# Kernel optimization log

Hardware: AMD Instinct MI355X
Metric: run time of the kernel (lower is better)

The kernel has to match this reference:

```python
import jax, jax.numpy as jnp
import numpy as np

SIGMA = 2.5
NEIGH_THRESH = 8.0
COORD_SCALE = 40.0  # Angstrom-scale box so the 8A cutoff gives realistic sparsity


def _rbf_weights(vs, vg):
    # vs: [B, Ns, 3], vg: [B, Ng, 3] -> [B, Ns, Ng] row-normalized gaussian RBF
    d2 = (jnp.sum(vs * vs, -1)[:, :, None]
          + jnp.sum(vg * vg, -1)[:, None, :]
          - 2.0 * jnp.einsum('bnd,bmd->bnm', vs, vg))
    d2 = jnp.maximum(d2, 0.0)
    w = jnp.exp(-d2 / (SIGMA ** 2)) * (d2 < NEIGH_THRESH ** 2)
    return w / (jnp.sum(w, -1, keepdims=True) + 1e-8)


def setup_inputs() -> dict:
    key = jax.random.key(0)
    ks = jax.random.split(key, 12)
    B, Ns, Ng, D = 4, 16384, 2048, 128
    s = 1.0 / np.sqrt(D)
    sp = 1.0 / np.sqrt(2 * D)
    return {
        'xs': jax.random.normal(ks[0], (B, Ns, D), jnp.float32),
        'xg': jax.random.normal(ks[1], (B, Ng, D), jnp.float32),
        'vs': jax.random.uniform(ks[2], (B, Ns, 3), jnp.float32) * COORD_SCALE,
        'vg': jax.random.uniform(ks[3], (B, Ng, 3), jnp.float32) * COORD_SCALE,
        'Ws_pre': jax.random.normal(ks[4], (D, D), jnp.float32) * s,
        'bs_pre': jnp.zeros((D,), jnp.float32),
        'Wg_pre': jax.random.normal(ks[5], (D, D), jnp.float32) * s,
        'bg_pre': jnp.zeros((D,), jnp.float32),
        'Ws_post': jax.random.normal(ks[6], (2 * D, D), jnp.float32) * sp,
        'bs_post': jnp.zeros((D,), jnp.float32),
        'Wg_post': jax.random.normal(ks[7], (2 * D, D), jnp.float32) * sp,
        'bg_post': jnp.zeros((D,), jnp.float32),
    }


def reference(xs, xg, vs, vg, Ws_pre, bs_pre, Wg_pre, bg_pre,
              Ws_post, bs_post, Wg_post, bg_post):
    # pre-encoders (surface.x = s_pre_block(surface.x); graph.x = g_pre_block(graph.x))
    xs_h = jax.nn.relu(jnp.einsum('bnd,de->bne', xs, Ws_pre) + bs_pre)
    xg_h = jax.nn.relu(jnp.einsum('bmd,de->bme', xg, Wg_pre) + bg_pre)
    # RBF bipartite message passing (non-BP path): xs_out = rbf_w @ graph.x; xg_out = rbf_w.T @ surface.x
    w = _rbf_weights(vs, vg)                                  # [B, Ns, Ng]
    xs_out = jnp.einsum('bnm,bmd->bnd', w, xg_h)              # graph -> surface
    xg_out = jnp.einsum('bnm,bnd->bmd', w, xs_h)              # surface -> graph
    # post blocks fuse old features with messages
    xs_new = jax.nn.relu(jnp.einsum('bnd,de->bne',
                                    jnp.concatenate([xs_h, xs_out], -1), Ws_post) + bs_post)
    xg_new = jax.nn.relu(jnp.einsum('bmd,de->bme',
                                    jnp.concatenate([xg_h, xg_out], -1), Wg_post) + bg_post)
    # concat along node dim so output is a single array: [B, Ns+Ng, D]
    return jnp.concatenate([xs_new, xg_new], axis=1)
```

## Files before the change

kernel.cpp:

```cpp
#include <hip/hip_runtime.h>
#include <hip/hip_bf16.h>

#define BB 4
#define NS 16384
#define NG 2048
#define DD 128
#define SPLITG 16
#define C2 (-0.23083120f)

typedef short bf16x8 __attribute__((ext_vector_type(8)));
typedef unsigned short u16x8 __attribute__((ext_vector_type(8)));
typedef float f32x4 __attribute__((ext_vector_type(4)));
typedef float f32x16 __attribute__((ext_vector_type(16)));
typedef int i32x4 __attribute__((ext_vector_type(4)));

#if __has_builtin(__builtin_amdgcn_exp2f)
#define EXP2(x) __builtin_amdgcn_exp2f(x)
#else
#define EXP2(x) exp2f(x)
#endif

__device__ __forceinline__ unsigned short f2bf(float x) {
  unsigned int u = __builtin_bit_cast(unsigned int, x);
  u += 0x7FFFu + ((u >> 16) & 1u);
  return (unsigned short)(u >> 16);
}
__device__ __forceinline__ float bf2f(unsigned short h) {
  unsigned int u = ((unsigned int)h) << 16;
  return __builtin_bit_cast(float, u);
}

#define PACK_SWAP(e0, e1, e2, e3, e4, e5, e6, e7, OUT)                       \
  {                                                                          \
    unsigned pq0, pq1, pq2, pq3;                                             \
    asm("v_cvt_pk_bf16_f32 %0, %1, %2" : "=v"(pq0) : "v"(e0), "v"(e1));      \
    asm("v_cvt_pk_bf16_f32 %0, %1, %2" : "=v"(pq1) : "v"(e2), "v"(e3));      \
    asm("v_cvt_pk_bf16_f32 %0, %1, %2" : "=v"(pq2) : "v"(e4), "v"(e5));      \
    asm("v_cvt_pk_bf16_f32 %0, %1, %2" : "=v"(pq3) : "v"(e6), "v"(e7));      \
    asm("v_permlane32_swap_b32 %0, %1" : "+v"(pq0), "+v"(pq2));              \
    asm("v_permlane32_swap_b32 %0, %1" : "+v"(pq1), "+v"(pq3));              \
    i32x4 tmp_ = {(int)pq0, (int)pq1, (int)pq2, (int)pq3};                   \
    OUT = __builtin_bit_cast(bf16x8, tmp_);                                  \
  }

__device__ __forceinline__ void posprep1(const float* __restrict__ v, int i,
                                         unsigned short* __restrict__ pos1,
                                         unsigned short* __restrict__ pos2) {
  float x = v[i * 3 + 0], y = v[i * 3 + 1], z = v[i * 3 + 2];
  unsigned short hx = f2bf(x), hy = f2bf(y), hz = f2bf(z);
  float fx = bf2f(hx), fy = bf2f(hy), fz = bf2f(hz);
  unsigned short lx = f2bf(x - fx), ly = f2bf(y - fy), lz = f2bf(z - fz);
  float n = x * x + y * y + z * z;
  unsigned short nh = f2bf(n);
  unsigned short nl = f2bf(n - bf2f(nh));
  unsigned short m2hx = f2bf(-2.f * fx), m2hy = f2bf(-2.f * fy),
                 m2hz = f2bf(-2.f * fz);
  unsigned short m2lx = f2bf(-2.f * bf2f(lx)), m2ly = f2bf(-2.f * bf2f(ly)),
                 m2lz = f2bf(-2.f * bf2f(lz));
  const unsigned short one = 0x3F80;
  u16x8 a0 = {m2hx, m2hy, m2hz, m2lx, m2ly, m2lz, m2hx, m2hy};
  u16x8 a1 = {m2hz, m2lx, m2ly, m2lz, nh, nl, one, one};
  u16x8 b0 = {hx, hy, hz, hx, hy, hz, lx, ly};
  u16x8 b1 = {lz, lx, ly, lz, one, one, nh, nl};
  *(u16x8*)(pos1 + (long)i * 16) = a0;
  *(u16x8*)(pos1 + (long)i * 16 + 8) = a1;
  *(u16x8*)(pos2 + (long)i * 16) = b0;
  *(u16x8*)(pos2 + (long)i * 16 + 8) = b1;
}

__global__ __launch_bounds__(256) void prep_k(
    const float* __restrict__ vs, const float* __restrict__ vg,
    const float* __restrict__ Ws_pre, const float* __restrict__ Wg_pre,
    const float* __restrict__ Ws_post, const float* __restrict__ Wg_post,
    unsigned short* __restrict__ pos1_s, unsigned short* __restrict__ pos2_s,
    unsigned short* __restrict__ pos1_g, unsigned short* __restrict__ pos2_g,
    unsigned short* __restrict__ WtS_pre, unsigned short* __restrict__ WtG_pre,
    unsigned short* __restrict__ WtS_post,
    unsigned short* __restrict__ WtG_post) {
  const int NODEBLK = (BB * (NS + NG)) / 256;
  int bid = blockIdx.x, tid = threadIdx.x;
  if (bid < NODEBLK) {
    int i = bid * 256 + tid;
    if (i < BB * NS)
      posprep1(vs, i, pos1_s, pos2_s);
    else
      posprep1(vg, i - BB * NS, pos1_g, pos2_g);
  } else {
    int k2 = (bid - NODEBLK) * 256 + tid;
    const float* W;
    unsigned short* Wt;
    int kshift, loc;
    if (k2 < 16384) { W = Ws_pre; Wt = WtS_pre; kshift = 7; loc = k2; }
    else if (k2 < 32768) { W = Wg_pre; Wt = WtG_pre; kshift = 7; loc = k2 - 16384; }
    else if (k2 < 65536) { W = Ws_post; Wt = WtS_post; kshift = 8; loc = k2 - 32768; }
    else { W = Wg_post; Wt = WtG_post; kshift = 8; loc = k2 - 65536; }
    int K = 1 << kshift;
    int e = loc >> kshift, k = loc & (K - 1);
    Wt[(long)e * K + k] = f2bf(W[(long)k * 128 + e]);
  }
}

__global__ __launch_bounds__(256) void pre_mfma_k(
    const float* __restrict__ xs, const float* __restrict__ xg,
    const unsigned short* __restrict__ WtS,
    const unsigned short* __restrict__ WtG, const float* __restrict__ bs,
    const float* __restrict__ bg, unsigned short* __restrict__ xs_h,
    unsigned short* __restrict__ xg_h) {
  long r0 = (long)blockIdx.x * 64;
  const float* X;
  const unsigned short* Wt;
  const float* bias;
  unsigned short* H;
  long row0;
  if (r0 < (long)BB * NS) {
    X = xs; Wt = WtS; bias = bs; H = xs_h; row0 = r0;
  } else {
    X = xg; Wt = WtG; bias = bg; H = xg_h; row0 = r0 - (long)BB * NS;
  }
  int tid = threadIdx.x, l = tid & 63, w = tid >> 6;
  int g = l >> 4, r = l & 15;
  row0 += w * 16;
  const float* xrow = X + (row0 + r) * DD;
  f32x4 z4 = {0.f, 0.f, 0.f, 0.f};
  f32x4 acc[8];
#pragma unroll
  for (int i = 0; i < 8; ++i) acc[i] = z4;
#pragma unroll
  for (int ks = 0; ks < 4; ++ks) {
    float4 v0 = *(const float4*)(xrow + ks * 32 + 8 * g);
    float4 v1 = *(const float4*)(xrow + ks * 32 + 8 * g + 4);
    bf16x8 a;
    a[0] = (short)f2bf(v0.x); a[1] = (short)f2bf(v0.y);
    a[2] = (short)f2bf(v0.z); a[3] = (short)f2bf(v0.w);
    a[4] = (short)f2bf(v1.x); a[5] = (short)f2bf(v1.y);
    a[6] = (short)f2bf(v1.z); a[7] = (short)f2bf(v1.w);
#pragma unroll
    for (int ct = 0; ct < 8; ++ct) {
      bf16x8 b = *reinterpret_cast<const bf16x8*>(Wt + (ct * 16 + r) * DD +
                                                  ks * 32 + 8 * g);
      acc[ct] = __builtin_amdgcn_mfma_f32_16x16x32_bf16(a, b, acc[ct], 0, 0, 0);
    }
  }
#pragma unroll
  for (int ct = 0; ct < 8; ++ct) {
    float bv = bias[ct * 16 + r];
#pragma unroll
    for (int r4 = 0; r4 < 4; ++r4) {
      long row = row0 + 4 * g + r4;
      H[row * DD + ct * 16 + r] = f2bf(fmaxf(acc[ct][r4] + bv, 0.f));
    }
  }
}

__global__ __launch_bounds__(256) void transpose_k(
    const unsigned short* __restrict__ H, unsigned short* __restrict__ HT,
    int R, const float* __restrict__ scale) {
  __shared__ unsigned short lds[64 * 136];
  int tid = threadIdx.x;
  long r0 = (long)blockIdx.x * 64;
#pragma unroll
  for (int q = 0; q < 4; ++q) {
    int idx = q * 2048 + tid * 8;
    int rr = idx >> 7, cc = idx & 127;
    u16x8 v = *reinterpret_cast<const u16x8*>(H + (r0 + rr) * 128 + cc);
    if (scale) {
      float s = scale[r0 + rr];
#pragma unroll
      for (int i = 0; i < 8; ++i) v[i] = f2bf(bf2f(v[i]) * s);
    }
    *(u16x8*)&lds[rr * 136 + cc] = v;
  }
  __syncthreads();
  int e = tid >> 1, half = tid & 1;
#pragma unroll
  for (int q = 0; q < 4; ++q) {
    u16x8 v;
#pragma unroll
    for (int i = 0; i < 8; ++i)
      v[i] = lds[(half * 32 + q * 8 + i) * 136 + e];
    *reinterpret_cast<u16x8*>(HT + (long)e * R + r0 + half * 32 + q * 8) = v;
  }
}

__global__ __launch_bounds__(256) void msg_s_k(
    const unsigned short* __restrict__ pos1_g,
    const unsigned short* __restrict__ pos2_s,
    const unsigned short* __restrict__ xg_hT, unsigned short* __restrict__ xs_o,
    float* __restrict__ rsinv) {
  __shared__ __align__(16) unsigned short ldsB[2][128 * 64];
  const int tid = threadIdx.x;
  const int w = tid >> 6, l = tid & 63;
  const int ln = l & 31, hi = l >> 5;
  const int b = blockIdx.y;
  const long bNS = (long)b * NS, bNG = (long)b * NG;
  const long row0 = (long)blockIdx.x * 128 + w * 32;
  const long BNG = (long)BB * NG;
  const int NCH = NG / 64;

  const bf16x8 bP = *reinterpret_cast<const bf16x8*>(
      pos2_s + (bNS + row0 + ln) * 16 + 8 * hi);

  const f32x16 zz = {0.f, 0.f, 0.f, 0.f, 0.f, 0.f, 0.f, 0.f,
                     0.f, 0.f, 0.f, 0.f, 0.f, 0.f, 0.f, 0.f};
  f32x16 acc[4] = {zz, zz, zz, zz};
  float rs0 = 0.f, rs1 = 0.f, rs2 = 0.f, rs3 = 0.f;

  const int tf = tid >> 3;
  const int tsp = tid & 7;
  const unsigned short* p0 = xg_hT + (long)(0 * 32 + tf) * BNG + bNG +
                             (tsp ^ (tf & 7)) * 8;
  const unsigned short* p1 = p0 + (long)32 * BNG;
  const unsigned short* p2 = p0 + (long)64 * BNG;
  const unsigned short* p3 = p0 + (long)96 * BNG;
  const unsigned short* pp = pos1_g + (bNG + ln) * 16 + 8 * hi;

  u16x8 stA[4];
  bf16x8 pA0, pA1, pA0n, pA1n;
  stA[0] = *reinterpret_cast<const u16x8*>(p0);
  stA[1] = *reinterpret_cast<const u16x8*>(p1);
  stA[2] = *reinterpret_cast<const u16x8*>(p2);
  stA[3] = *reinterpret_cast<const u16x8*>(p3);
#pragma unroll
  for (int q = 0; q < 4; ++q)
    *(u16x8*)&ldsB[0][(q * 32 + tf) * 64 + tsp * 8] = stA[q];
  stA[0] = *reinterpret_cast<const u16x8*>(p0 + 64);
  stA[1] = *reinterpret_cast<const u16x8*>(p1 + 64);
  stA[2] = *reinterpret_cast<const u16x8*>(p2 + 64);
  stA[3] = *reinterpret_cast<const u16x8*>(p3 + 64);
  p0 += 128; p1 += 128; p2 += 128; p3 += 128;
  pA0 = *reinterpret_cast<const bf16x8*>(pp);
  pA1 = *reinterpret_cast<const bf16x8*>(pp + 32 * 16);
  pA0n = *reinterpret_cast<const bf16x8*>(pp + 64 * 16);
  pA1n = *reinterpret_cast<const bf16x8*>(pp + 96 * 16);
  pp += 128 * 16;
  __syncthreads();

#pragma unroll 1
  for (int c = 0; c < NCH; ++c) {
    const int buf = c & 1;
    float ex[2][16];
    bf16x8 fr[2][2];
#pragma unroll
    for (int t2 = 0; t2 < 2; ++t2) {
      f32x16 S = __builtin_amdgcn_mfma_f32_32x32x16_bf16(t2 ? pA1 : pA0, bP,
                                                         zz, 0, 0, 0);
#pragma unroll
      for (int r = 0; r < 16; ++r) ex[t2][r] = EXP2(S[r] * C2);
      PACK_SWAP(ex[t2][0], ex[t2][1], ex[t2][2], ex[t2][3], ex[t2][4],
                ex[t2][5], ex[t2][6], ex[t2][7], fr[t2][0]);
      PACK_SWAP(ex[t2][8], ex[t2][9], ex[t2][10], ex[t2][11], ex[t2][12],
                ex[t2][13], ex[t2][14], ex[t2][15], fr[t2][1]);
    }
#pragma unroll
    for (int r = 0; r < 4; ++r) {
      rs0 += ex[0][r] + ex[1][r];
      rs1 += ex[0][r + 4] + ex[1][r + 4];
      rs2 += ex[0][r + 8] + ex[1][r + 8];
      rs3 += ex[0][r + 12] + ex[1][r + 12];
    }
#pragma unroll
    for (int t2 = 0; t2 < 2; ++t2) {
#pragma unroll
      for (int kh = 0; kh < 2; ++kh) {
        const int kt = t2 * 2 + kh;
        const int spr = ((kt * 2 + hi) ^ (ln & 7)) * 8;
#pragma unroll
        for (int nt = 0; nt < 4; ++nt) {
          const bf16x8 bm = *reinterpret_cast<const bf16x8*>(
              &ldsB[buf][(nt * 32 + ln) * 64 + spr]);
          acc[nt] = __builtin_amdgcn_mfma_f32_32x32x16_bf16(fr[t2][kh], bm,
                                                            acc[nt], 0, 0, 0);
        }
      }
    }
    if (c + 1 < NCH) {
#pragma unroll
      for (int q = 0; q < 4; ++q)
        *(u16x8*)&ldsB[buf ^ 1][(q * 32 + tf) * 64 + tsp * 8] = stA[q];
    }
    if (c + 2 < NCH) {
      stA[0] = *reinterpret_cast<const u16x8*>(p0);
      stA[1] = *reinterpret_cast<const u16x8*>(p1);
      stA[2] = *reinterpret_cast<const u16x8*>(p2);
      stA[3] = *reinterpret_cast<const u16x8*>(p3);
      p0 += 64; p1 += 64; p2 += 64; p3 += 64;
    }
    pA0 = pA0n;
    pA1 = pA1n;
    if (c + 2 < NCH) {
      pA0n = *reinterpret_cast<const bf16x8*>(pp);
      pA1n = *reinterpret_cast<const bf16x8*>(pp + 32 * 16);
      pp += 64 * 16;
    }
    __syncthreads();
  }

  float rtot = (rs0 + rs1) + (rs2 + rs3);
  rtot += __shfl_xor(rtot, 32, 64);
  float denom = rtot + 1e-8f;
  float rsi = 1.f / denom;
  if (hi == 0) rsinv[bNS + row0 + ln] = rsi;
#pragma unroll
  for (int r = 0; r < 16; ++r) {
    const int crow = (r & 3) + 8 * (r >> 2) + 4 * hi;
    float rsib = __shfl(rsi, crow, 64);
    long rowg = bNS + row0 + crow;
#pragma unroll
    for (int nt = 0; nt < 4; ++nt)
      xs_o[rowg * DD + nt * 32 + ln] = f2bf(acc[nt][r] * rsib);
  }
}

__global__ __launch_bounds__(256) void msg_g_k(
    const unsigned short* __restrict__ pos1_s,
    const unsigned short* __restrict__ pos2_g,
    const unsigned short* __restrict__ xs_hT, unsigned short* __restrict__ part) {
  __shared__ __align__(16) unsigned short ldsB[2][128 * 64];
  const int tid = threadIdx.x;
  const int w = tid >> 6, l = tid & 63;
  const int ln = l & 31, hi = l >> 5;
  const int b = blockIdx.y, spz = blockIdx.z;
  const long bNS = (long)b * NS, bNG = (long)b * NG;
  const long nbeg = (long)spz * (NS / SPLITG);
  const long row0 = (long)blockIdx.x * 128 + w * 32;
  const long BNS = (long)BB * NS;
  const int NCH = (NS / SPLITG) / 64;

  const bf16x8 bP = *reinterpret_cast<const bf16x8*>(
      pos2_g + (bNG + row0 + ln) * 16 + 8 * hi);

  const f32x16 zz = {0.f, 0.f, 0.f, 0.f, 0.f, 0.f, 0.f, 0.f,
                     0.f, 0.f, 0.f, 0.f, 0.f, 0.f, 0.f, 0.f};
  f32x16 acc[4] = {zz, zz, zz, zz};

  const int tf = tid >> 3;
  const int tsp = tid & 7;
  const unsigned short* p0 = xs_hT + (long)(0 * 32 + tf) * BNS + bNS + nbeg +
                             (tsp ^ (tf & 7)) * 8;
  const unsigned short* p1 = p0 + (long)32 * BNS;
  const unsigned short* p2 = p0 + (long)64 * BNS;
  const unsigned short* p3 = p0 + (long)96 * BNS;
  const unsigned short* pp = pos1_s + (bNS + nbeg + ln) * 16 + 8 * hi;

  u16x8 stA[4];
  bf16x8 pA0, pA1, pA0n, pA1n;
  stA[0] = *reinterpret_cast<const u16x8*>(p0);
  stA[1] = *reinterpret_cast<const u16x8*>(p1);
  stA[2] = *reinterpret_cast<const u16x8*>(p2);
  stA[3] = *reinterpret_cast<const u16x8*>(p3);
#pragma unroll
  for (int q = 0; q < 4; ++q)
    *(u16x8*)&ldsB[0][(q * 32 + tf) * 64 + tsp * 8] = stA[q];
  stA[0] = *reinterpret_cast<const u16x8*>(p0 + 64);
  stA[1] = *reinterpret_cast<const u16x8*>(p1 + 64);
  stA[2] = *reinterpret_cast<const u16x8*>(p2 + 64);
  stA[3] = *reinterpret_cast<const u16x8*>(p3 + 64);
  p0 += 128; p1 += 128; p2 += 128; p3 += 128;
  pA0 = *reinterpret_cast<const bf16x8*>(pp);
  pA1 = *reinterpret_cast<const bf16x8*>(pp + 32 * 16);
  pA0n = *reinterpret_cast<const bf16x8*>(pp + 64 * 16);
  pA1n = *reinterpret_cast<const bf16x8*>(pp + 96 * 16);
  pp += 128 * 16;
  __syncthreads();

#pragma unroll 1
  for (int c = 0; c < NCH; ++c) {
    const int buf = c & 1;
    float ex[2][16];
    bf16x8 fr[2][2];
#pragma unroll
    for (int t2 = 0; t2 < 2; ++t2) {
      f32x16 S = __builtin_amdgcn_mfma_f32_32x32x16_bf16(t2 ? pA1 : pA0, bP,
                                                         zz, 0, 0, 0);
#pragma unroll
      for (int r = 0; r < 16; ++r) ex[t2][r] = EXP2(S[r] * C2);
      PACK_SWAP(ex[t2][0], ex[t2][1], ex[t2][2], ex[t2][3], ex[t2][4],
                ex[t2][5], ex[t2][6], ex[t2][7], fr[t2][0]);
      PACK_SWAP(ex[t2][8], ex[t2][9], ex[t2][10], ex[t2][11], ex[t2][12],
                ex[t2][13], ex[t2][14], ex[t2][15], fr[t2][1]);
    }
#pragma unroll
    for (int t2 = 0; t2 < 2; ++t2) {
#pragma unroll
      for (int kh = 0; kh < 2; ++kh) {
        const int kt = t2 * 2 + kh;
        const int spr = ((kt * 2 + hi) ^ (ln & 7)) * 8;
#pragma unroll
        for (int nt = 0; nt < 4; ++nt) {
          const bf16x8 bm = *reinterpret_cast<const bf16x8*>(
              &ldsB[buf][(nt * 32 + ln) * 64 + spr]);
          acc[nt] = __builtin_amdgcn_mfma_f32_32x32x16_bf16(fr[t2][kh], bm,
                                                            acc[nt], 0, 0, 0);
        }
      }
    }
    if (c + 1 < NCH) {
#pragma unroll
      for (int q = 0; q < 4; ++q)
        *(u16x8*)&ldsB[buf ^ 1][(q * 32 + tf) * 64 + tsp * 8] = stA[q];
    }
    if (c + 2 < NCH) {
      stA[0] = *reinterpret_cast<const u16x8*>(p0);
      stA[1] = *reinterpret_cast<const u16x8*>(p1);
      stA[2] = *reinterpret_cast<const u16x8*>(p2);
      stA[3] = *reinterpret_cast<const u16x8*>(p3);
      p0 += 64; p1 += 64; p2 += 64; p3 += 64;
    }
    pA0 = pA0n;
    pA1 = pA1n;
    if (c + 2 < NCH) {
      pA0n = *reinterpret_cast<const bf16x8*>(pp);
      pA1n = *reinterpret_cast<const bf16x8*>(pp + 32 * 16);
      pp += 64 * 16;
    }
    __syncthreads();
  }

  const long pbase = (long)spz * BB * NG;
#pragma unroll
  for (int r = 0; r < 16; ++r) {
    const int crow = (r & 3) + 8 * (r >> 2) + 4 * hi;
    long rowg = pbase + bNG + row0 + crow;
#pragma unroll
    for (int nt = 0; nt < 4; ++nt)
      part[rowg * DD + nt * 32 + ln] = f2bf(acc[nt][r]);
  }
}

__global__ __launch_bounds__(256) void reduce_k(
    const unsigned short* __restrict__ part, unsigned short* __restrict__ xg_o) {
  long i = ((long)blockIdx.x * 256 + threadIdx.x) * 8;
  const long S = (long)BB * NG * DD;
  float a[8];
#pragma unroll
  for (int k = 0; k < 8; ++k) a[k] = 0.f;
#pragma unroll
  for (int s = 0; s < SPLITG; ++s) {
    u16x8 v = *reinterpret_cast<const u16x8*>(part + s * S + i);
#pragma unroll
    for (int k = 0; k < 8; ++k) a[k] += bf2f(v[k]);
  }
  u16x8 o;
#pragma unroll
  for (int k = 0; k < 8; ++k) o[k] = f2bf(a[k]);
  *reinterpret_cast<u16x8*>(xg_o + i) = o;
}

__global__ __launch_bounds__(256) void post_mfma_k(
    const unsigned short* __restrict__ Ha, const unsigned short* __restrict__ Hb,
    const unsigned short* __restrict__ Wt, const float* __restrict__ bias,
    float* __restrict__ out, int shift, int mask, int off) {
  int tid = threadIdx.x, l = tid & 63, w = tid >> 6;
  int g = l >> 4, r = l & 15;
  long row0 = (long)blockIdx.x * 64 + w * 16;
  const unsigned short* ha = Ha + (row0 + r) * DD;
  const unsigned short* hb = Hb + (row0 + r) * DD;
  f32x4 z4 = {0.f, 0.f, 0.f, 0.f};
  f32x4 acc[8];
#pragma unroll
  for (int i = 0; i < 8; ++i) acc[i] = z4;
#pragma unroll
  for (int ks = 0; ks < 8; ++ks) {
    const unsigned short* src = (ks < 4) ? (ha + ks * 32) : (hb + (ks - 4) * 32);
    bf16x8 a = *reinterpret_cast<const bf16x8*>(src + 8 * g);
#pragma unroll
    for (int ct = 0; ct < 8; ++ct) {
      bf16x8 b = *reinterpret_cast<const bf16x8*>(Wt + (ct * 16 + r) * 256 +
                                                  ks * 32 + 8 * g);
      acc[ct] = __builtin_amdgcn_mfma_f32_16x16x32_bf16(a, b, acc[ct], 0, 0, 0);
    }
  }
#pragma unroll
  for (int ct = 0; ct < 8; ++ct) {
    float bv = bias[ct * 16 + r];
#pragma unroll
    for (int r4 = 0; r4 < 4; ++r4) {
      long rowg = row0 + 4 * g + r4;
      long bb = rowg >> shift;
      long n = rowg & mask;
      out[(bb * (NS + NG) + off + n) * DD + ct * 16 + r] =
          fmaxf(acc[ct][r4] + bv, 0.f);
    }
  }
}

extern "C" void kernel_launch(void* const* d_in, const int* in_sizes, int n_in,
                              void* d_out, int out_size, void* d_ws,
                              size_t ws_size, hipStream_t stream) {
  const float* xs = (const float*)d_in[0];
  const float* xg = (const float*)d_in[1];
  const float* vs = (const float*)d_in[2];
  const float* vg = (const float*)d_in[3];
  const float* Ws_pre = (const float*)d_in[4];
  const float* bs_pre = (const float*)d_in[5];
  const float* Wg_pre = (const float*)d_in[6];
  const float* bg_pre = (const float*)d_in[7];
  const float* Ws_post = (const float*)d_in[8];
  const float* bs_post = (const float*)d_in[9];
  const float* Wg_post = (const float*)d_in[10];
  const float* bg_post = (const float*)d_in[11];
  float* out = (float*)d_out;

  char* p = (char*)d_ws;
  unsigned short* pos1_s = (unsigned short*)p; p += (size_t)BB * NS * 16 * 2;
  unsigned short* pos2_s = (unsigned short*)p; p += (size_t)BB * NS * 16 * 2;
  unsigned short* pos1_g = (unsigned short*)p; p += (size_t)BB * NG * 16 * 2;
  unsigned short* pos2_g = (unsigned short*)p; p += (size_t)BB * NG * 16 * 2;
  unsigned short* WtS_pre = (unsigned short*)p; p += (size_t)128 * 128 * 2;
  unsigned short* WtG_pre = (unsigned short*)p; p += (size_t)128 * 128 * 2;
  unsigned short* WtS_post = (unsigned short*)p; p += (size_t)128 * 256 * 2;
  unsigned short* WtG_post = (unsigned short*)p; p += (size_t)128 * 256 * 2;
  unsigned short* xg_h = (unsigned short*)p; p += (size_t)BB * NG * DD * 2;
  unsigned short* xg_hT = (unsigned short*)p; p += (size_t)BB * NG * DD * 2;
  unsigned short* xs_hT = (unsigned short*)p; p += (size_t)BB * NS * DD * 2;
  unsigned short* xg_o = (unsigned short*)p; p += (size_t)BB * NG * DD * 2;
  float* rsinv = (float*)p; p += (size_t)BB * NS * 4;
  unsigned short* xs_h = (unsigned short*)p;
  unsigned short* xs_o = xs_h + (size_t)BB * NS * DD;
  unsigned short* part = xs_h;
  p += (size_t)2 * BB * NS * DD * 2;

  prep_k<<<(BB * (NS + NG)) / 256 + 98304 / 256, 256, 0, stream>>>(
      vs, vg, Ws_pre, Wg_pre, Ws_post, Wg_post, pos1_s, pos2_s, pos1_g,
      pos2_g, WtS_pre, WtG_pre, WtS_post, WtG_post);
  pre_mfma_k<<<(BB * NS + BB * NG) / 64, 256, 0, stream>>>(
      xs, xg, WtS_pre, WtG_pre, bs_pre, bg_pre, xs_h, xg_h);
  transpose_k<<<BB * NG / 64, 256, 0, stream>>>(xg_h, xg_hT, BB * NG, nullptr);
  msg_s_k<<<dim3(NS / 128, BB), 256, 0, stream>>>(pos1_g, pos2_s, xg_hT, xs_o,
                                                  rsinv);
  transpose_k<<<BB * NS / 64, 256, 0, stream>>>(xs_h, xs_hT, BB * NS, rsinv);
  post_mfma_k<<<BB * NS / 64, 256, 0, stream>>>(xs_h, xs_o, WtS_post, bs_post,
                                                out, 14, NS - 1, 0);
  msg_g_k<<<dim3(NG / 128, BB, SPLITG), 256, 0, stream>>>(pos1_s, pos2_g,
                                                          xs_hT, part);
  reduce_k<<<(BB * NG * DD) / 8 / 256, 256, 0, stream>>>(part, xg_o);
  post_mfma_k<<<BB * NG / 64, 256, 0, stream>>>(xg_h, xg_o, WtG_post, bg_post,
                                                out, 11, NG - 1, NS);
}
```

Before: 198.4 us.

## Split surface message kernel over graph dimension with combine pass

Splits msg_s_k's loop over the graph nodes into two z-slices. Each slice writes unnormalized bf16 partial messages and partial row sums, and a new combine kernel adds the two halves and applies the normalization. The goal is more blocks in flight and shorter per-block serial loops, which should improve GPU occupancy and latency hiding. The cost is an extra kernel launch plus an extra global read/write pass over the surface message buffer, and the partials are rounded to bf16 before being summed.

```diff
diff --git a/kernel.cpp b/kernel.cpp
--- a/kernel.cpp
+++ b/kernel.cpp
@@ -6,7 +6,8 @@
 #define NG 2048
 #define DD 128
 #define SPLITG 16
-#define C2 (-0.23083120f)
+#define SPLITS 2
+#define C2F (-0.23083120f)
 
 typedef short bf16x8 __attribute__((ext_vector_type(8)));
 typedef unsigned short u16x8 __attribute__((ext_vector_type(8)));
@@ -185,17 +186,19 @@
 __global__ __launch_bounds__(256) void msg_s_k(
     const unsigned short* __restrict__ pos1_g,
     const unsigned short* __restrict__ pos2_s,
-    const unsigned short* __restrict__ xg_hT, unsigned short* __restrict__ xs_o,
-    float* __restrict__ rsinv) {
+    const unsigned short* __restrict__ xg_hT,
+    unsigned short* __restrict__ part0, unsigned short* __restrict__ part1,
+    float* __restrict__ rs_part) {
   __shared__ __align__(16) unsigned short ldsB[2][128 * 64];
   const int tid = threadIdx.x;
   const int w = tid >> 6, l = tid & 63;
   const int ln = l & 31, hi = l >> 5;
-  const int b = blockIdx.y;
+  const int b = blockIdx.y, spz = blockIdx.z;
   const long bNS = (long)b * NS, bNG = (long)b * NG;
+  const long nbeg = (long)spz * (NG / SPLITS);
   const long row0 = (long)blockIdx.x * 128 + w * 32;
   const long BNG = (long)BB * NG;
-  const int NCH = NG / 64;
+  const int NCH = (NG / SPLITS) / 64;
 
   const bf16x8 bP = *reinterpret_cast<const bf16x8*>(
       pos2_s + (bNS + row0 + ln) * 16 + 8 * hi);
@@ -207,12 +210,12 @@
 
   const int tf = tid >> 3;
   const int tsp = tid & 7;
-  const unsigned short* p0 = xg_hT + (long)(0 * 32 + tf) * BNG + bNG +
+  const unsigned short* p0 = xg_hT + (long)tf * BNG + bNG + nbeg +
                              (tsp ^ (tf & 7)) * 8;
   const unsigned short* p1 = p0 + (long)32 * BNG;
   const unsigned short* p2 = p0 + (long)64 * BNG;
   const unsigned short* p3 = p0 + (long)96 * BNG;
-  const unsigned short* pp = pos1_g + (bNG + ln) * 16 + 8 * hi;
+  const unsigned short* pp = pos1_g + (bNG + nbeg + ln) * 16 + 8 * hi;
 
   u16x8 stA[4];
   bf16x8 pA0, pA1, pA0n, pA1n;
@@ -245,7 +248,7 @@
       f32x16 S = __builtin_amdgcn_mfma_f32_32x32x16_bf16(t2 ? pA1 : pA0, bP,
                                                          zz, 0, 0, 0);
 #pragma unroll
-      for (int r = 0; r < 16; ++r) ex[t2][r] = EXP2(S[r] * C2);
+      for (int r = 0; r < 16; ++r) ex[t2][r] = EXP2(S[r] * C2F);
       PACK_SWAP(ex[t2][0], ex[t2][1], ex[t2][2], ex[t2][3], ex[t2][4],
                 ex[t2][5], ex[t2][6], ex[t2][7], fr[t2][0]);
       PACK_SWAP(ex[t2][8], ex[t2][9], ex[t2][10], ex[t2][11], ex[t2][12],
@@ -295,20 +298,34 @@
     __syncthreads();
   }
 
-  float rtot = (rs0 + rs1) + (rs2 + rs3);
-  rtot += __shfl_xor(rtot, 32, 64);
-  float denom = rtot + 1e-8f;
-  float rsi = 1.f / denom;
-  if (hi == 0) rsinv[bNS + row0 + ln] = rsi;
+  float rsp = (rs0 + rs1) + (rs2 + rs3);
+  rsp += __shfl_xor(rsp, 32, 64);
+  if (hi == 0) rs_part[(long)spz * (BB * NS) + bNS + row0 + ln] = rsp;
+  unsigned short* dst = spz ? part1 : part0;
 #pragma unroll
   for (int r = 0; r < 16; ++r) {
     const int crow = (r & 3) + 8 * (r >> 2) + 4 * hi;
-    float rsib = __shfl(rsi, crow, 64);
     long rowg = bNS + row0 + crow;
 #pragma unroll
     for (int nt = 0; nt < 4; ++nt)
-      xs_o[rowg * DD + nt * 32 + ln] = f2bf(acc[nt][r] * rsib);
-  }
+      dst[rowg * DD + nt * 32 + ln] = f2bf(acc[nt][r]);
+  }
+}
+
+__global__ __launch_bounds__(256) void combine_s_k(
+    const unsigned short* __restrict__ part1, const float* __restrict__ rs_part,
+    unsigned short* __restrict__ xs_o, float* __restrict__ rsinv) {
+  long i = ((long)blockIdx.x * 256 + threadIdx.x) * 8;
+  long row = i >> 7;
+  float s = rs_part[row] + rs_part[(long)BB * NS + row] + 1e-8f;
+  float ri = 1.f / s;
+  u16x8 a = *reinterpret_cast<const u16x8*>(xs_o + i);
+  u16x8 bq = *reinterpret_cast<const u16x8*>(part1 + i);
+  u16x8 o;
+#pragma unroll
+  for (int k = 0; k < 8; ++k) o[k] = f2bf((bf2f(a[k]) + bf2f(bq[k])) * ri);
+  *reinterpret_cast<u16x8*>(xs_o + i) = o;
+  if ((i & 127) == 0) rsinv[row] = ri;
 }
 
 __global__ __launch_bounds__(256) void msg_g_k(
@@ -335,7 +352,7 @@
 
   const int tf = tid >> 3;
   const int tsp = tid & 7;
-  const unsigned short* p0 = xs_hT + (long)(0 * 32 + tf) * BNS + bNS + nbeg +
+  const unsigned short* p0 = xs_hT + (long)tf * BNS + bNS + nbeg +
                              (tsp ^ (tf & 7)) * 8;
   const unsigned short* p1 = p0 + (long)32 * BNS;
   const unsigned short* p2 = p0 + (long)64 * BNS;
@@ -373,7 +390,7 @@
       f32x16 S = __builtin_amdgcn_mfma_f32_32x32x16_bf16(t2 ? pA1 : pA0, bP,
                                                          zz, 0, 0, 0);
 #pragma unroll
-      for (int r = 0; r < 16; ++r) ex[t2][r] = EXP2(S[r] * C2);
+      for (int r = 0; r < 16; ++r) ex[t2][r] = EXP2(S[r] * C2F);
       PACK_SWAP(ex[t2][0], ex[t2][1], ex[t2][2], ex[t2][3], ex[t2][4],
                 ex[t2][5], ex[t2][6], ex[t2][7], fr[t2][0]);
       PACK_SWAP(ex[t2][8], ex[t2][9], ex[t2][10], ex[t2][11], ex[t2][12],
@@ -513,11 +530,13 @@
   unsigned short* xg_h = (unsigned short*)p; p += (size_t)BB * NG * DD * 2;
   unsigned short* xg_hT = (unsigned short*)p; p += (size_t)BB * NG * DD * 2;
   unsigned short* xs_hT = (unsigned short*)p; p += (size_t)BB * NS * DD * 2;
+  unsigned short* part1 = xs_hT;
   unsigned short* xg_o = (unsigned short*)p; p += (size_t)BB * NG * DD * 2;
   float* rsinv = (float*)p; p += (size_t)BB * NS * 4;
+  float* rs_part = (float*)p; p += (size_t)SPLITS * BB * NS * 4;
   unsigned short* xs_h = (unsigned short*)p;
   unsigned short* xs_o = xs_h + (size_t)BB * NS * DD;
-  unsigned short* part = xs_h;
+  unsigned short* part_g = xs_h;
   p += (size_t)2 * BB * NS * DD * 2;
 
   prep_k<<<(BB * (NS + NG)) / 256 + 98304 / 256, 256, 0, stream>>>(
@@ -526,14 +545,16 @@
   pre_mfma_k<<<(BB * NS + BB * NG) / 64, 256, 0, stream>>>(
       xs, xg, WtS_pre, WtG_pre, bs_pre, bg_pre, xs_h, xg_h);
   transpose_k<<<BB * NG / 64, 256, 0, stream>>>(xg_h, xg_hT, BB * NG, nullptr);
-  msg_s_k<<<dim3(NS / 128, BB), 256, 0, stream>>>(pos1_g, pos2_s, xg_hT, xs_o,
-                                                  rsinv);
+  msg_s_k<<<dim3(NS / 128, BB, SPLITS), 256, 0, stream>>>(
+      pos1_g, pos2_s, xg_hT, xs_o, part1, rs_part);
+  combine_s_k<<<(BB * NS * DD) / 8 / 256, 256, 0, stream>>>(part1, rs_part,
+                                                            xs_o, rsinv);
   transpose_k<<<BB * NS / 64, 256, 0, stream>>>(xs_h, xs_hT, BB * NS, rsinv);
   post_mfma_k<<<BB * NS / 64, 256, 0, stream>>>(xs_h, xs_o, WtS_post, bs_post,
                                                 out, 14, NS - 1, 0);
   msg_g_k<<<dim3(NG / 128, BB, SPLITG), 256, 0, stream>>>(pos1_s, pos2_g,
-                                                          xs_hT, part);
-  reduce_k<<<(BB * NG * DD) / 8 / 256, 256, 0, stream>>>(part, xg_o);
+                                                          xs_hT, part_g);
+  reduce_k<<<(BB * NG * DD) / 8 / 256, 256, 0, stream>>>(part_g, xg_o);
   post_mfma_k<<<BB * NG / 64, 256, 0, stream>>>(xg_h, xg_o, WtG_post, bg_post,
                                                 out, 11, NG - 1, NS);
 }
```

Measured after the change: 205.9 us. +3.8%, slower.

## Software-pipeline RBF weight computation one chunk ahead of aggregation MFMAs

Applied to the files above, without the earlier changes.

In both message-passing kernels, the distance MFMA, exp2 and bf16 packing for the next chunk now run interleaved with the aggregation MFMAs of the current chunk. The current chunk's fragments come from a prologue that computes the first chunk before the loop. This lets exp/VALU work overlap the matrix-core work instead of serialising with it. The pack-and-permlane sequence is also merged into one asm block with explicit s_nop hazards, and position loads now go straight from global memory each iteration instead of being double-buffered in registers. This raises register pressure and adds load latency to the critical path.

```diff
diff --git a/kernel.cpp b/kernel.cpp
--- a/kernel.cpp
+++ b/kernel.cpp
@@ -6,7 +6,7 @@
 #define NG 2048
 #define DD 128
 #define SPLITG 16
-#define C2 (-0.23083120f)
+#define C2F (-0.23083120f)
 
 typedef short bf16x8 __attribute__((ext_vector_type(8)));
 typedef unsigned short u16x8 __attribute__((ext_vector_type(8)));
@@ -30,17 +30,22 @@
   return __builtin_bit_cast(float, u);
 }
 
-#define PACK_SWAP(e0, e1, e2, e3, e4, e5, e6, e7, OUT)                       \
-  {                                                                          \
-    unsigned pq0, pq1, pq2, pq3;                                             \
-    asm("v_cvt_pk_bf16_f32 %0, %1, %2" : "=v"(pq0) : "v"(e0), "v"(e1));      \
-    asm("v_cvt_pk_bf16_f32 %0, %1, %2" : "=v"(pq1) : "v"(e2), "v"(e3));      \
-    asm("v_cvt_pk_bf16_f32 %0, %1, %2" : "=v"(pq2) : "v"(e4), "v"(e5));      \
-    asm("v_cvt_pk_bf16_f32 %0, %1, %2" : "=v"(pq3) : "v"(e6), "v"(e7));      \
-    asm("v_permlane32_swap_b32 %0, %1" : "+v"(pq0), "+v"(pq2));              \
-    asm("v_permlane32_swap_b32 %0, %1" : "+v"(pq1), "+v"(pq3));              \
-    i32x4 tmp_ = {(int)pq0, (int)pq1, (int)pq2, (int)pq3};                   \
-    OUT = __builtin_bit_cast(bf16x8, tmp_);                                  \
+#define PACK_SWAP(e0, e1, e2, e3, e4, e5, e6, e7, OUT)                        \
+  {                                                                           \
+    unsigned pq0, pq1, pq2, pq3;                                              \
+    asm("v_cvt_pk_bf16_f32 %0, %4, %5\n\t"                                    \
+        "v_cvt_pk_bf16_f32 %1, %6, %7\n\t"                                    \
+        "v_cvt_pk_bf16_f32 %2, %8, %9\n\t"                                    \
+        "v_cvt_pk_bf16_f32 %3, %10, %11\n\t"                                  \
+        "s_nop 1\n\t"                                                         \
+        "v_permlane32_swap_b32 %0, %2\n\t"                                    \
+        "v_permlane32_swap_b32 %1, %3\n\t"                                    \
+        "s_nop 1"                                                             \
+        : "=&v"(pq0), "=&v"(pq1), "=&v"(pq2), "=&v"(pq3)                      \
+        : "v"(e0), "v"(e1), "v"(e2), "v"(e3), "v"(e4), "v"(e5), "v"(e6),      \
+          "v"(e7));                                                           \
+    i32x4 tmp_ = {(int)pq0, (int)pq1, (int)pq2, (int)pq3};                    \
+    OUT = __builtin_bit_cast(bf16x8, tmp_);                                   \
   }
 
 __device__ __forceinline__ void posprep1(const float* __restrict__ v, int i,
@@ -207,15 +212,13 @@
 
   const int tf = tid >> 3;
   const int tsp = tid & 7;
-  const unsigned short* p0 = xg_hT + (long)(0 * 32 + tf) * BNG + bNG +
-                             (tsp ^ (tf & 7)) * 8;
+  const unsigned short* p0 = xg_hT + (long)tf * BNG + bNG + (tsp ^ (tf & 7)) * 8;
   const unsigned short* p1 = p0 + (long)32 * BNG;
   const unsigned short* p2 = p0 + (long)64 * BNG;
   const unsigned short* p3 = p0 + (long)96 * BNG;
   const unsigned short* pp = pos1_g + (bNG + ln) * 16 + 8 * hi;
 
   u16x8 stA[4];
-  bf16x8 pA0, pA1, pA0n, pA1n;
   stA[0] = *reinterpret_cast<const u16x8*>(p0);
   stA[1] = *reinterpret_cast<const u16x8*>(p1);
   stA[2] = *reinterpret_cast<const u16x8*>(p2);
@@ -228,55 +231,100 @@
   stA[2] = *reinterpret_cast<const u16x8*>(p2 + 64);
   stA[3] = *reinterpret_cast<const u16x8*>(p3 + 64);
   p0 += 128; p1 += 128; p2 += 128; p3 += 128;
-  pA0 = *reinterpret_cast<const bf16x8*>(pp);
-  pA1 = *reinterpret_cast<const bf16x8*>(pp + 32 * 16);
-  pA0n = *reinterpret_cast<const bf16x8*>(pp + 64 * 16);
-  pA1n = *reinterpret_cast<const bf16x8*>(pp + 96 * 16);
-  pp += 128 * 16;
+
+  bf16x8 frC0, frC1, frC2, frC3;
+  {
+    bf16x8 a0 = *reinterpret_cast<const bf16x8*>(pp);
+    f32x16 S = __builtin_amdgcn_mfma_f32_32x32x16_bf16(a0, bP, zz, 0, 0, 0);
+    float ex[16];
+#pragma unroll
+    for (int r = 0; r < 16; ++r) ex[r] = EXP2(S[r] * C2F);
+#pragma unroll
+    for (int r = 0; r < 4; ++r) {
+      rs0 += ex[r]; rs1 += ex[r + 4]; rs2 += ex[r + 8]; rs3 += ex[r + 12];
+    }
+    PACK_SWAP(ex[0], ex[1], ex[2], ex[3], ex[4], ex[5], ex[6], ex[7], frC0);
+    PACK_SWAP(ex[8], ex[9], ex[10], ex[11], ex[12], ex[13], ex[14], ex[15],
+              frC1);
+    bf16x8 a1 = *reinterpret_cast<const bf16x8*>(pp + 32 * 16);
+    S = __builtin_amdgcn_mfma_f32_32x32x16_bf16(a1, bP, zz, 0, 0, 0);
+#pragma unroll
+    for (int r = 0; r < 16; ++r) ex[r] = EXP2(S[r] * C2F);
+#pragma unroll
+    for (int r = 0; r < 4; ++r) {
+      rs0 += ex[r]; rs1 += ex[r + 4]; rs2 += ex[r + 8]; rs3 += ex[r + 12];
+    }
+    PACK_SWAP(ex[0], ex[1], ex[2], ex[3], ex[4], ex[5], ex[6], ex[7], frC2);
+    PACK_SWAP(ex[8], ex[9], ex[10], ex[11], ex[12], ex[13], ex[14], ex[15],
+              frC3);
+  }
   __syncthreads();
 
 #pragma unroll 1
   for (int c = 0; c < NCH; ++c) {
     const int buf = c & 1;
-    float ex[2][16];
-    bf16x8 fr[2][2];
-#pragma unroll
-    for (int t2 = 0; t2 < 2; ++t2) {
-      f32x16 S = __builtin_amdgcn_mfma_f32_32x32x16_bf16(t2 ? pA1 : pA0, bP,
-                                                         zz, 0, 0, 0);
-#pragma unroll
-      for (int r = 0; r < 16; ++r) ex[t2][r] = EXP2(S[r] * C2);
-      PACK_SWAP(ex[t2][0], ex[t2][1], ex[t2][2], ex[t2][3], ex[t2][4],
-                ex[t2][5], ex[t2][6], ex[t2][7], fr[t2][0]);
-      PACK_SWAP(ex[t2][8], ex[t2][9], ex[t2][10], ex[t2][11], ex[t2][12],
-                ex[t2][13], ex[t2][14], ex[t2][15], fr[t2][1]);
-    }
-#pragma unroll
-    for (int r = 0; r < 4; ++r) {
-      rs0 += ex[0][r] + ex[1][r];
-      rs1 += ex[0][r + 4] + ex[1][r + 4];
-      rs2 += ex[0][r + 8] + ex[1][r + 8];
-      rs3 += ex[0][r + 12] + ex[1][r + 12];
-    }
-#pragma unroll
-    for (int t2 = 0; t2 < 2; ++t2) {
-#pragma unroll
-      for (int kh = 0; kh < 2; ++kh) {
-        const int kt = t2 * 2 + kh;
-        const int spr = ((kt * 2 + hi) ^ (ln & 7)) * 8;
-#pragma unroll
-        for (int nt = 0; nt < 4; ++nt) {
-          const bf16x8 bm = *reinterpret_cast<const bf16x8*>(
-              &ldsB[buf][(nt * 32 + ln) * 64 + spr]);
-          acc[nt] = __builtin_amdgcn_mfma_f32_32x32x16_bf16(fr[t2][kh], bm,
-                                                            acc[nt], 0, 0, 0);
-        }
+    const bool haveN = (c + 1 < NCH);
+    bf16x8 frN0, frN1, frN2, frN3;
+    f32x16 S;
+    if (haveN) {
+      bf16x8 a0 =
+          *reinterpret_cast<const bf16x8*>(pp + (long)(c + 1) * 1024);
+      S = __builtin_amdgcn_mfma_f32_32x32x16_bf16(a0, bP, zz, 0, 0, 0);
+    }
+#pragma unroll
+    for (int kt = 0; kt < 2; ++kt) {
+      const bf16x8 fA = kt ? frC1 : frC0;
+      const int spr = ((kt * 2 + hi) ^ (ln & 7)) * 8;
+#pragma unroll
+      for (int nt = 0; nt < 4; ++nt) {
+        const bf16x8 bm = *reinterpret_cast<const bf16x8*>(
+            &ldsB[buf][(nt * 32 + ln) * 64 + spr]);
+        acc[nt] =
+            __builtin_amdgcn_mfma_f32_32x32x16_bf16(fA, bm, acc[nt], 0, 0, 0);
       }
     }
-    if (c + 1 < NCH) {
+    if (haveN) {
+      float ex[16];
+#pragma unroll
+      for (int r = 0; r < 16; ++r) ex[r] = EXP2(S[r] * C2F);
+#pragma unroll
+      for (int r = 0; r < 4; ++r) {
+        rs0 += ex[r]; rs1 += ex[r + 4]; rs2 += ex[r + 8]; rs3 += ex[r + 12];
+      }
+      PACK_SWAP(ex[0], ex[1], ex[2], ex[3], ex[4], ex[5], ex[6], ex[7], frN0);
+      PACK_SWAP(ex[8], ex[9], ex[10], ex[11], ex[12], ex[13], ex[14], ex[15],
+                frN1);
+      bf16x8 a1 = *reinterpret_cast<const bf16x8*>(pp + (long)(c + 1) * 1024 +
+                                                   32 * 16);
+      S = __builtin_amdgcn_mfma_f32_32x32x16_bf16(a1, bP, zz, 0, 0, 0);
+    }
+#pragma unroll
+    for (int kt = 2; kt < 4; ++kt) {
+      const bf16x8 fA = (kt == 2) ? frC2 : frC3;
+      const int spr = ((kt * 2 + hi) ^ (ln & 7)) * 8;
+#pragma unroll
+      for (int nt = 0; nt < 4; ++nt) {
+        const bf16x8 bm = *reinterpret_cast<const bf16x8*>(
+            &ldsB[buf][(nt * 32 + ln) * 64 + spr]);
+        acc[nt] =
+            __builtin_amdgcn_mfma_f32_32x32x16_bf16(fA, bm, acc[nt], 0, 0, 0);
+      }
+    }
+    if (haveN) {
+      float ex[16];
+#pragma unroll
+      for (int r = 0; r < 16; ++r) ex[r] = EXP2(S[r] * C2F);
+#pragma unroll
+      for (int r = 0; r < 4; ++r) {
+        rs0 += ex[r]; rs1 += ex[r + 4]; rs2 += ex[r + 8]; rs3 += ex[r + 12];
+      }
+      PACK_SWAP(ex[0], ex[1], ex[2], ex[3], ex[4], ex[5], ex[6], ex[7], frN2);
+      PACK_SWAP(ex[8], ex[9], ex[10], ex[11], ex[12], ex[13], ex[14], ex[15],
+                frN3);
 #pragma unroll
       for (int q = 0; q < 4; ++q)
         *(u16x8*)&ldsB[buf ^ 1][(q * 32 + tf) * 64 + tsp * 8] = stA[q];
+      frC0 = frN0; frC1 = frN1; frC2 = frN2; frC3 = frN3;
     }
     if (c + 2 < NCH) {
       stA[0] = *reinterpret_cast<const u16x8*>(p0);
@@ -284,13 +332,6 @@
       stA[2] = *reinterpret_cast<const u16x8*>(p2);
       stA[3] = *reinterpret_cast<const u16x8*>(p3);
       p0 += 64; p1 += 64; p2 += 64; p3 += 64;
-    }
-    pA0 = pA0n;
-    pA1 = pA1n;
-    if (c + 2 < NCH) {
-      pA0n = *reinterpret_cast<const bf16x8*>(pp);
-      pA1n = *reinterpret_cast<const bf16x8*>(pp + 32 * 16);
-      pp += 64 * 16;
     }
     __syncthreads();
   }
@@ -335,7 +376,7 @@
 
   const int tf = tid >> 3;
   const int tsp = tid & 7;
-  const unsigned short* p0 = xs_hT + (long)(0 * 32 + tf) * BNS + bNS + nbeg +
+  const unsigned short* p0 = xs_hT + (long)tf * BNS + bNS + nbeg +
                              (tsp ^ (tf & 7)) * 8;
   const unsigned short* p1 = p0 + (long)32 * BNS;
   const unsigned short* p2 = p0 + (long)64 * BNS;
@@ -343,7 +384,6 @@
   const unsigned short* pp = pos1_s + (bNS + nbeg + ln) * 16 + 8 * hi;
 
   u16x8 stA[4];
-  bf16x8 pA0, pA1, pA0n, pA1n;
   stA[0] = *reinterpret_cast<const u16x8*>(p0);
   stA[1] = *reinterpret_cast<const u16x8*>(p1);
   stA[2] = *reinterpret_cast<const u16x8*>(p2);
@@ -356,48 +396,84 @@
   stA[2] = *reinterpret_cast<const u16x8*>(p2 + 64);
   stA[3] = *reinterpret_cast<const u16x8*>(p3 + 64);
   p0 += 128; p1 += 128; p2 += 128; p3 += 128;
-  pA0 = *reinterpret_cast<const bf16x8*>(pp);
-  pA1 = *reinterpret_cast<const bf16x8*>(pp + 32 * 16);
-  pA0n = *reinterpret_cast<const bf16x8*>(pp + 64 * 16);
-  pA1n = *reinterpret_cast<const bf16x8*>(pp + 96 * 16);
-  pp += 128 * 16;
+
+  bf16x8 frC0, frC1, frC2, frC3;
+  {
+    bf16x8 a0 = *reinterpret_cast<const bf16x8*>(pp);
+    f32x16 S = __builtin_amdgcn_mfma_f32_32x32x16_bf16(a0, bP, zz, 0, 0, 0);
+    float ex[16];
+#pragma unroll
+    for (int r = 0; r < 16; ++r) ex[r] = EXP2(S[r] * C2F);
+    PACK_SWAP(ex[0], ex[1], ex[2], ex[3], ex[4], ex[5], ex[6], ex[7], frC0);
+    PACK_SWAP(ex[8], ex[9], ex[10], ex[11], ex[12], ex[13], ex[14], ex[15],
+              frC1);
+    bf16x8 a1 = *reinterpret_cast<const bf16x8*>(pp + 32 * 16);
+    S = __builtin_amdgcn_mfma_f32_32x32x16_bf16(a1, bP, zz, 0, 0, 0);
+#pragma unroll
+    for (int r = 0; r < 16; ++r) ex[r] = EXP2(S[r] * C2F);
+    PACK_SWAP(ex[0], ex[1], ex[2], ex[3], ex[4], ex[5], ex[6], ex[7], frC2);
+    PACK_SWAP(ex[8], ex[9], ex[10], ex[11], ex[12], ex[13], ex[14], ex[15],
+              frC3);
+  }
   __syncthreads();
 
 #pragma unroll 1
   for (int c = 0; c < NCH; ++c) {
     const int buf = c & 1;
-    float ex[2][16];
-    bf16x8 fr[2][2];
-#pragma unroll
-    for (int t2 = 0; t2 < 2; ++t2) {
-      f32x16 S = __builtin_amdgcn_mfma_f32_32x32x16_bf16(t2 ? pA1 : pA0, bP,
-                                                         zz, 0, 0, 0);
-#pragma unroll
-      for (int r = 0; r < 16; ++r) ex[t2][r] = EXP2(S[r] * C2);
-      PACK_SWAP(ex[t2][0], ex[t2][1], ex[t2][2], ex[t2][3], ex[t2][4],
-                ex[t2][5], ex[t2][6], ex[t2][7], fr[t2][0]);
-      PACK_SWAP(ex[t2][8], ex[t2][9], ex[t2][10], ex[t2][11], ex[t2][12],
-                ex[t2][13], ex[t2][14], ex[t2][15], fr[t2][1]);
-    }
-#pragma unroll
-    for (int t2 = 0; t2 < 2; ++t2) {
-#pragma unroll
-      for (int kh = 0; kh < 2; ++kh) {
-        const int kt = t2 * 2 + kh;
-        const int spr = ((kt * 2 + hi) ^ (ln & 7)) * 8;
-#pragma unroll
-        for (int nt = 0; nt < 4; ++nt) {
-          const bf16x8 bm = *reinterpret_cast<const bf16x8*>(
-              &ldsB[buf][(nt * 32 + ln) * 64 + spr]);
-          acc[nt] = __builtin_amdgcn_mfma_f32_32x32x16_bf16(fr[t2][kh], bm,
-                                                            acc[nt], 0, 0, 0);
-        }
+    const bool haveN = (c + 1 < NCH);
+    bf16x8 frN0, frN1, frN2, frN3;
+    f32x16 S;
+    if (haveN) {
+      bf16x8 a0 =
+          *reinterpret_cast<const bf16x8*>(pp + (long)(c + 1) * 1024);
+      S = __builtin_amdgcn_mfma_f32_32x32x16_bf16(a0, bP, zz, 0, 0, 0);
+    }
+#pragma unroll
+    for (int kt = 0; kt < 2; ++kt) {
+      const bf16x8 fA = kt ? frC1 : frC0;
+      const int spr = ((kt * 2 + hi) ^ (ln & 7)) * 8;
+#pragma unroll
+      for (int nt = 0; nt < 4; ++nt) {
+        const bf16x8 bm = *reinterpret_cast<const bf16x8*>(
+            &ldsB[buf][(nt * 32 + ln) * 64 + spr]);
+        acc[nt] =
+            __builtin_amdgcn_mfma_f32_32x32x16_bf16(fA, bm, acc[nt], 0, 0, 0);
       }
     }
-    if (c + 1 < NCH) {
+    if (haveN) {
+      float ex[16];
+#pragma unroll
+      for (int r = 0; r < 16; ++r) ex[r] = EXP2(S[r] * C2F);
+      PACK_SWAP(ex[0], ex[1], ex[2], ex[3], ex[4], ex[5], ex[6], ex[7], frN0);
+      PACK_SWAP(ex[8], ex[9], ex[10], ex[11], ex[12], ex[13], ex[14], ex[15],
+                frN1);
+      bf16x8 a1 = *reinterpret_cast<const bf16x8*>(pp + (long)(c + 1) * 1024 +
+                                                   32 * 16);
+      S = __builtin_amdgcn_mfma_f32_32x32x16_bf16(a1, bP, zz, 0, 0, 0);
+    }
+#pragma unroll
+    for (int kt = 2; kt < 4; ++kt) {
+      const bf16x8 fA = (kt == 2) ? frC2 : frC3;
+      const int spr = ((kt * 2 + hi) ^ (ln & 7)) * 8;
+#pragma unroll
+      for (int nt = 0; nt < 4; ++nt) {
+        const bf16x8 bm = *reinterpret_cast<const bf16x8*>(
+            &ldsB[buf][(nt * 32 + ln) * 64 + spr]);
+        acc[nt] =
+            __builtin_amdgcn_mfma_f32_32x32x16_bf16(fA, bm, acc[nt], 0, 0, 0);
+      }
+    }
+    if (haveN) {
+      float ex[16];
+#pragma unroll
+      for (int r = 0; r < 16; ++r) ex[r] = EXP2(S[r] * C2F);
+      PACK_SWAP(ex[0], ex[1], ex[2], ex[3], ex[4], ex[5], ex[6], ex[7], frN2);
+      PACK_SWAP(ex[8], ex[9], ex[10], ex[11], ex[12], ex[13], ex[14], ex[15],
+                frN3);
 #pragma unroll
       for (int q = 0; q < 4; ++q)
         *(u16x8*)&ldsB[buf ^ 1][(q * 32 + tf) * 64 + tsp * 8] = stA[q];
+      frC0 = frN0; frC1 = frN1; frC2 = frN2; frC3 = frN3;
     }
     if (c + 2 < NCH) {
       stA[0] = *reinterpret_cast<const u16x8*>(p0);
@@ -405,13 +481,6 @@
       stA[2] = *reinterpret_cast<const u16x8*>(p2);
       stA[3] = *reinterpret_cast<const u16x8*>(p3);
       p0 += 64; p1 += 64; p2 += 64; p3 += 64;
-    }
-    pA0 = pA0n;
-    pA1 = pA1n;
-    if (c + 2 < NCH) {
-      pA0n = *reinterpret_cast<const bf16x8*>(pp);
-      pA1n = *reinterpret_cast<const bf16x8*>(pp + 32 * 16);
-      pp += 64 * 16;
     }
     __syncthreads();
   }
@@ -517,7 +586,7 @@
   float* rsinv = (float*)p; p += (size_t)BB * NS * 4;
   unsigned short* xs_h = (unsigned short*)p;
   unsigned short* xs_o = xs_h + (size_t)BB * NS * DD;
-  unsigned short* part = xs_h;
+  unsigned short* part_g = xs_h;
   p += (size_t)2 * BB * NS * DD * 2;
 
   prep_k<<<(BB * (NS + NG)) / 256 + 98304 / 256, 256, 0, stream>>>(
@@ -532,8 +601,8 @@
   post_mfma_k<<<BB * NS / 64, 256, 0, stream>>>(xs_h, xs_o, WtS_post, bs_post,
                                                 out, 14, NS - 1, 0);
   msg_g_k<<<dim3(NG / 128, BB, SPLITG), 256, 0, stream>>>(pos1_s, pos2_g,
-                                                          xs_hT, part);
-  reduce_k<<<(BB * NG * DD) / 8 / 256, 256, 0, stream>>>(part, xg_o);
+                                                          xs_hT, part_g);
+  reduce_k<<<(BB * NG * DD) / 8 / 256, 256, 0, stream>>>(part_g, xg_o);
   post_mfma_k<<<BB * NG / 64, 256, 0, stream>>>(xg_h, xg_o, WtG_post, bg_post,
                                                 out, 11, NG - 1, NS);
 }
```

Result: slower. 208.2 us (+4.9%).
